# Performance work log

Hardware: AMD Instinct MI355X
Metric: run time of the kernel (lower is better)

The kernel has to match this reference:

```python
import jax, jax.numpy as jnp
import numpy as np

K = 10  # knn neighbors
GF = 100  # gf_num = 25*4


def setup_inputs() -> dict:
    key = jax.random.key(0)
    ks = jax.random.split(key, 14)
    B, N = 4, 8192
    s = 0.1
    inp = {
        "x": jax.random.normal(ks[0], (B, N, 3), dtype=jnp.float32),
        # conv1: (3+K)->20->GF, 1x1 convs == per-point linears
        "w1a": jax.random.normal(ks[1], (3 + K, 20), jnp.float32) * s,
        "b1a": jax.random.normal(ks[2], (20,), jnp.float32) * s,
        "w1b": jax.random.normal(ks[3], (20, GF), jnp.float32) * s,
        "b1b": jax.random.normal(ks[4], (GF,), jnp.float32) * s,
        # conv2: GF->GF
        "w2": jax.random.normal(ks[5], (GF, GF), jnp.float32) * s,
        "b2": jax.random.normal(ks[6], (GF,), jnp.float32) * s,
        # conv3: 2*GF->20->10->2
        "w3a": jax.random.normal(ks[7], (2 * GF, 20), jnp.float32) * s,
        "b3a": jax.random.normal(ks[8], (20,), jnp.float32) * s,
        "w3b": jax.random.normal(ks[9], (20, 10), jnp.float32) * s,
        "b3b": jax.random.normal(ks[10], (10,), jnp.float32) * s,
        "w3c": jax.random.normal(ks[11], (10, 2), jnp.float32) * s,
        "b3c": jax.random.normal(ks[12], (2,), jnp.float32) * s,
    }
    return inp


def reference(x, w1a, b1a, w1b, b1b, w2, b2, w3a, b3a, w3b, b3b, w3c, b3c):
    # pairwise squared distances: [B, N, N]
    sq = jnp.sum(x * x, axis=-1)
    d = sq[:, :, None] + sq[:, None, :] - 2.0 * jnp.einsum("bnc,bmc->bnm", x, x)
    # k smallest distances per point, ascending order (matches torch topk largest=False)
    topk = -jax.lax.top_k(-d, K)[0]  # [B, N, K]
    h = jnp.concatenate([x, topk], axis=-1)  # [B, N, 3+K]
    # conv1 (1x1 convs == per-point linears)
    x1 = jax.nn.relu(jax.nn.relu(h @ w1a + b1a) @ w1b + b1b)  # [B, N, GF]
    # conv2
    x2 = jax.nn.relu(x1 @ w2 + b2)  # [B, N, GF]
    # global avg pool over points, broadcast back
    pool = jnp.mean(x2, axis=1, keepdims=True)  # [B, 1, GF]
    N = x1.shape[1]
    feat = jnp.concatenate([x1, jnp.broadcast_to(pool, (x1.shape[0], N, pool.shape[-1]))], axis=-1)
    # conv3 head + log-softmax over the 2 classes (torch dim=-2 on [B,2,N] layout)
    o = jax.nn.relu(feat @ w3a + b3a)
    o = jax.nn.relu(o @ w3b + b3b)
    o = o @ w3c + b3c  # [B, N, 2]
    return jax.nn.log_softmax(o, axis=-1)
```

## Files before the change

kernel.cpp:

```cpp
#include <hip/hip_runtime.h>
#include <math.h>

#define N_PTS   8192
#define NBATCH  4
#define NQ      (N_PTS*NBATCH)
#define GFN     100
#define KNN     10
#define NSPLIT  8
#define SPLITL  (N_PTS/NSPLIT)
#define MBLK    128
#define CHK     25

__device__ __forceinline__ float med3f(float a, float b, float c){
  return __builtin_amdgcn_fmed3f(a, b, c);
}

__device__ __forceinline__ void insert10(float (&m)[KNN], float d){
  #pragma unroll
  for (int k = KNN-1; k > 0; k--) m[k] = med3f(d, m[k-1], m[k]);
  m[0] = fminf(m[0], d);
}

__global__ __launch_bounds__(256) void knn_kernel(const float* __restrict__ x,
                                                  float* __restrict__ cand,
                                                  float* __restrict__ pool){
  __shared__ float4 tile[SPLITL];
  const int t  = threadIdx.x;
  const int qb = blockIdx.x;
  const int s  = blockIdx.y;
  const int q  = qb * 256 + t;
  const int b  = q >> 13;
  const float* xb = x + (size_t)b * N_PTS * 3;

  if (qb == 0 && s == 0){
    for (int i = t; i < NBATCH*GFN; i += 256) pool[i] = 0.0f;
  }

  #pragma unroll
  for (int k = 0; k < 4; k++){
    const int j = t + 256*k;
    const float* ps = xb + (size_t)(s*SPLITL + j)*3;
    float px = ps[0], py = ps[1], pz = ps[2];
    float sq = fmaf(pz, pz, fmaf(py, py, px*px));
    tile[j] = make_float4(px, py, pz, sq);
  }
  __syncthreads();

  const float xi = x[(size_t)q*3+0], yi = x[(size_t)q*3+1], zi = x[(size_t)q*3+2];
  const float sqi = fmaf(zi, zi, fmaf(yi, yi, xi*xi));

  float m[KNN];
  #pragma unroll
  for (int k = 0; k < KNN; k++) m[k] = INFINITY;

  #pragma unroll 8
  for (int j = 0; j < SPLITL; j++){
    float4 p = tile[j];
    float dot = fmaf(zi, p.z, fmaf(yi, p.y, xi*p.x));
    float d   = fmaf(-2.0f, dot, sqi + p.w);
    insert10(m, d);
  }

  #pragma unroll
  for (int k = 0; k < KNN; k++) cand[(size_t)(s*KNN + k)*NQ + q] = m[k];
}

__global__ __launch_bounds__(256) void mlp1_kernel(
    const float* __restrict__ x,   const float* __restrict__ cand,
    const float* __restrict__ w1a, const float* __restrict__ b1a,
    const float* __restrict__ w1b, const float* __restrict__ b1b,
    const float* __restrict__ w2,  const float* __restrict__ b2,
    float* __restrict__ x1t, float* __restrict__ pool){
  __shared__ float t20s[MBLK*21];
  __shared__ float x1s[MBLK*101];
  const int t = threadIdx.x;
  const int p = t & 63;
  const int g = __builtin_amdgcn_readfirstlane(t >> 6);
  const int q0 = blockIdx.x * MBLK;
  const int b  = q0 >> 13;

  if (g < 2){
    const int pr = g*64 + p;
    const int q  = q0 + pr;
    float m[KNN];
    #pragma unroll
    for (int k = 0; k < KNN; k++) m[k] = INFINITY;
    #pragma unroll
    for (int i = 0; i < NSPLIT*KNN; i++) insert10(m, cand[(size_t)i*NQ + q]);

    float h[13];
    h[0] = x[(size_t)q*3+0]; h[1] = x[(size_t)q*3+1]; h[2] = x[(size_t)q*3+2];
    #pragma unroll
    for (int k = 0; k < KNN; k++) h[3+k] = m[k];

    float a[20];
    #pragma unroll
    for (int o = 0; o < 20; o++) a[o] = b1a[o];
    #pragma unroll
    for (int c = 0; c < 13; c++){
      float hv = h[c];
      #pragma unroll
      for (int o = 0; o < 20; o++) a[o] = fmaf(hv, w1a[c*20+o], a[o]);
    }
    #pragma unroll
    for (int o = 0; o < 20; o++) t20s[pr*21 + o] = fmaxf(a[o], 0.0f);
  }
  __syncthreads();

  const int o0 = g * CHK;
  float accA[CHK], accB[CHK];

  #pragma unroll
  for (int k = 0; k < CHK; k++){ float bv = b1b[o0+k]; accA[k] = bv; accB[k] = bv; }
  #pragma unroll 4
  for (int c = 0; c < 20; c++){
    float ta = t20s[p*21 + c];
    float tb = t20s[(64+p)*21 + c];
    #pragma unroll
    for (int k = 0; k < CHK; k++){
      float w = w1b[c*GFN + o0 + k];
      accA[k] = fmaf(ta, w, accA[k]);
      accB[k] = fmaf(tb, w, accB[k]);
    }
  }
  #pragma unroll
  for (int k = 0; k < CHK; k++){
    float va = fmaxf(accA[k], 0.0f);
    float vb = fmaxf(accB[k], 0.0f);
    x1s[p*101 + o0 + k] = va;
    x1s[(64+p)*101 + o0 + k] = vb;
    x1t[(size_t)(o0+k)*NQ + q0 + p]      = va;
    x1t[(size_t)(o0+k)*NQ + q0 + 64 + p] = vb;
  }
  __syncthreads();

  #pragma unroll
  for (int k = 0; k < CHK; k++){ float bv = b2[o0+k]; accA[k] = bv; accB[k] = bv; }
  #pragma unroll 4
  for (int c = 0; c < GFN; c++){
    float xa = x1s[p*101 + c];
    float xb = x1s[(64+p)*101 + c];
    #pragma unroll
    for (int k = 0; k < CHK; k++){
      float w = w2[c*GFN + o0 + k];
      accA[k] = fmaf(xa, w, accA[k]);
      accB[k] = fmaf(xb, w, accB[k]);
    }
  }
  #pragma unroll
  for (int k = 0; k < CHK; k++){
    float va = fmaxf(accA[k], 0.0f);
    float vb = fmaxf(accB[k], 0.0f);
    #pragma unroll
    for (int off = 1; off < 64; off <<= 1){
      va += __shfl_xor(va, off);
      vb += __shfl_xor(vb, off);
    }
    if (p == 0){
      atomicAdd(&pool[b*GFN + o0 + k], va);
      atomicAdd(&pool[b*GFN + o0 + k], vb);
    }
  }
}

__global__ __launch_bounds__(128) void head_kernel(
    const float* __restrict__ x1t, const float* __restrict__ pool,
    const float* __restrict__ w3a, const float* __restrict__ b3a,
    const float* __restrict__ w3b, const float* __restrict__ b3b,
    const float* __restrict__ w3c, const float* __restrict__ b3c,
    float* __restrict__ out){
  __shared__ float poolm[GFN];
  __shared__ float poolpart[20];
  const int t = threadIdx.x;
  const int q = blockIdx.x * 128 + t;
  const int b = q >> 13;

  if (t < GFN) poolm[t] = pool[b*GFN+t] * (1.0f / (float)N_PTS);
  __syncthreads();
  if (t < 20){
    float a = b3a[t];
    for (int c = 0; c < GFN; c++) a = fmaf(poolm[c], w3a[(GFN+c)*20+t], a);
    poolpart[t] = a;
  }
  __syncthreads();

  float acc[20];
  #pragma unroll
  for (int o = 0; o < 20; o++) acc[o] = 0.0f;
  #pragma unroll 8
  for (int c = 0; c < GFN; c++){
    float xv = x1t[(size_t)c*NQ + q];
    #pragma unroll
    for (int o = 0; o < 20; o++) acc[o] = fmaf(xv, w3a[c*20+o], acc[o]);
  }
  float o1[20];
  #pragma unroll
  for (int o = 0; o < 20; o++) o1[o] = fmaxf(acc[o] + poolpart[o], 0.0f);

  float o2[10];
  #pragma unroll
  for (int o = 0; o < 10; o++){
    float a = b3b[o];
    #pragma unroll
    for (int c = 0; c < 20; c++) a = fmaf(o1[c], w3b[c*10+o], a);
    o2[o] = fmaxf(a, 0.0f);
  }
  float e0 = b3c[0], e1 = b3c[1];
  #pragma unroll
  for (int c = 0; c < 10; c++){
    e0 = fmaf(o2[c], w3c[c*2+0], e0);
    e1 = fmaf(o2[c], w3c[c*2+1], e1);
  }
  float mx = fmaxf(e0, e1);
  float a0 = e0 - mx, a1 = e1 - mx;
  float lse = logf(expf(a0) + expf(a1));
  float2 r; r.x = a0 - lse; r.y = a1 - lse;
  *reinterpret_cast<float2*>(out + (size_t)q*2) = r;
}

extern "C" void kernel_launch(void* const* d_in, const int* in_sizes, int n_in,
                              void* d_out, int out_size, void* d_ws, size_t ws_size,
                              hipStream_t stream) {
  const float* x   = (const float*)d_in[0];
  const float* w1a = (const float*)d_in[1];
  const float* b1a = (const float*)d_in[2];
  const float* w1b = (const float*)d_in[3];
  const float* b1b = (const float*)d_in[4];
  const float* w2  = (const float*)d_in[5];
  const float* b2  = (const float*)d_in[6];
  const float* w3a = (const float*)d_in[7];
  const float* b3a = (const float*)d_in[8];
  const float* w3b = (const float*)d_in[9];
  const float* b3b = (const float*)d_in[10];
  const float* w3c = (const float*)d_in[11];
  const float* b3c = (const float*)d_in[12];
  float* out = (float*)d_out;

  char* ws = (char*)d_ws;
  float* cand = (float*)ws;
  float* x1t  = (float*)(ws + (size_t)NQ*NSPLIT*KNN*4);
  float* pool = (float*)(ws + (size_t)NQ*NSPLIT*KNN*4
                            + (size_t)GFN*NQ*4);

  knn_kernel<<<dim3(NQ/256, NSPLIT), 256, 0, stream>>>(x, cand, pool);
  mlp1_kernel<<<NQ/MBLK, 256, 0, stream>>>(x, cand, w1a, b1a, w1b, b1b, w2, b2, x1t, pool);
  head_kernel<<<NQ/128, 128, 0, stream>>>(x1t, pool, w3a, b3a, w3b, b3b, w3c, b3c, out);
}
```

Before: 273.3 us.

## Register-block KNN queries, widen MLP block, store x1 row-major for head

The KNN kernel now has each thread handle 4 query points against a shared tile, so every LDS load of a reference point is reused four times. The split count doubles to 16 so the grid stays large. The MLP kernel runs 512 threads, one point per thread-row with software-prefetched w2 weights, and writes x1 row-major so the head kernel can read it with float4 loads. The costs are more registers per thread in KNN (40 running minima), twice the candidate buffer traffic, and a longer merge loop in the MLP kernel.

```diff
diff --git a/kernel.cpp b/kernel.cpp
--- a/kernel.cpp
+++ b/kernel.cpp
@@ -6,10 +6,10 @@
 #define NQ      (N_PTS*NBATCH)
 #define GFN     100
 #define KNN     10
-#define NSPLIT  8
+#define NSPLIT  16
 #define SPLITL  (N_PTS/NSPLIT)
+#define QPL     4
 #define MBLK    128
-#define CHK     25
 
 __device__ __forceinline__ float med3f(float a, float b, float c){
   return __builtin_amdgcn_fmed3f(a, b, c);
@@ -25,52 +25,68 @@
                                                   float* __restrict__ cand,
                                                   float* __restrict__ pool){
   __shared__ float4 tile[SPLITL];
-  const int t  = threadIdx.x;
-  const int qb = blockIdx.x;
-  const int s  = blockIdx.y;
-  const int q  = qb * 256 + t;
-  const int b  = q >> 13;
+  const int t   = threadIdx.x;
+  const int w   = t >> 6;
+  const int p   = t & 63;
+  const int s   = blockIdx.y;
+  const int qb0 = blockIdx.x * 1024;
+  const int b   = qb0 >> 13;
   const float* xb = x + (size_t)b * N_PTS * 3;
 
-  if (qb == 0 && s == 0){
+  if (blockIdx.x == 0 && s == 0){
     for (int i = t; i < NBATCH*GFN; i += 256) pool[i] = 0.0f;
   }
 
   #pragma unroll
-  for (int k = 0; k < 4; k++){
+  for (int k = 0; k < 2; k++){
     const int j = t + 256*k;
     const float* ps = xb + (size_t)(s*SPLITL + j)*3;
     float px = ps[0], py = ps[1], pz = ps[2];
-    float sq = fmaf(pz, pz, fmaf(py, py, px*px));
-    tile[j] = make_float4(px, py, pz, sq);
-  }
-  __syncthreads();
-
-  const float xi = x[(size_t)q*3+0], yi = x[(size_t)q*3+1], zi = x[(size_t)q*3+2];
-  const float sqi = fmaf(zi, zi, fmaf(yi, yi, xi*xi));
-
-  float m[KNN];
-  #pragma unroll
-  for (int k = 0; k < KNN; k++) m[k] = INFINITY;
-
-  #pragma unroll 8
+    tile[j] = make_float4(px, py, pz, fmaf(pz, pz, fmaf(py, py, px*px)));
+  }
+  __syncthreads();
+
+  float qx[QPL], qy[QPL], qz[QPL], qs[QPL];
+  #pragma unroll
+  for (int u = 0; u < QPL; u++){
+    const int q = qb0 + w*256 + u*64 + p;
+    qx[u] = x[(size_t)q*3+0];
+    qy[u] = x[(size_t)q*3+1];
+    qz[u] = x[(size_t)q*3+2];
+    qs[u] = fmaf(qz[u], qz[u], fmaf(qy[u], qy[u], qx[u]*qx[u]));
+  }
+
+  float m[QPL][KNN];
+  #pragma unroll
+  for (int u = 0; u < QPL; u++)
+    #pragma unroll
+    for (int k = 0; k < KNN; k++) m[u][k] = INFINITY;
+
+  #pragma unroll 4
   for (int j = 0; j < SPLITL; j++){
-    float4 p = tile[j];
-    float dot = fmaf(zi, p.z, fmaf(yi, p.y, xi*p.x));
-    float d   = fmaf(-2.0f, dot, sqi + p.w);
-    insert10(m, d);
-  }
-
-  #pragma unroll
-  for (int k = 0; k < KNN; k++) cand[(size_t)(s*KNN + k)*NQ + q] = m[k];
-}
-
-__global__ __launch_bounds__(256) void mlp1_kernel(
+    float4 pt = tile[j];
+    #pragma unroll
+    for (int u = 0; u < QPL; u++){
+      float dot = fmaf(qz[u], pt.z, fmaf(qy[u], pt.y, qx[u]*pt.x));
+      float d   = fmaf(-2.0f, dot, qs[u] + pt.w);
+      insert10(m[u], d);
+    }
+  }
+
+  #pragma unroll
+  for (int u = 0; u < QPL; u++){
+    const int q = qb0 + w*256 + u*64 + p;
+    #pragma unroll
+    for (int k = 0; k < KNN; k++) cand[(size_t)(s*KNN + k)*NQ + q] = m[u][k];
+  }
+}
+
+__global__ __launch_bounds__(512) void mlp1_kernel(
     const float* __restrict__ x,   const float* __restrict__ cand,
     const float* __restrict__ w1a, const float* __restrict__ b1a,
     const float* __restrict__ w1b, const float* __restrict__ b1b,
     const float* __restrict__ w2,  const float* __restrict__ b2,
-    float* __restrict__ x1t, float* __restrict__ pool){
+    float* __restrict__ x1r, float* __restrict__ pool){
   __shared__ float t20s[MBLK*21];
   __shared__ float x1s[MBLK*101];
   const int t = threadIdx.x;
@@ -85,7 +101,7 @@
     float m[KNN];
     #pragma unroll
     for (int k = 0; k < KNN; k++) m[k] = INFINITY;
-    #pragma unroll
+    #pragma unroll 4
     for (int i = 0; i < NSPLIT*KNN; i++) insert10(m, cand[(size_t)i*NQ + q]);
 
     float h[13];
@@ -107,64 +123,61 @@
   }
   __syncthreads();
 
-  const int o0 = g * CHK;
-  float accA[CHK], accB[CHK];
-
-  #pragma unroll
-  for (int k = 0; k < CHK; k++){ float bv = b1b[o0+k]; accA[k] = bv; accB[k] = bv; }
-  #pragma unroll 4
+  const int half = g >> 2;
+  const int ph   = half*64 + p;
+  const int q    = q0 + ph;
+  const int o0   = (g & 3) * 25;
+
+  float acc[25];
+
+  #pragma unroll
+  for (int k = 0; k < 25; k++) acc[k] = b1b[o0+k];
+  #pragma unroll 1
   for (int c = 0; c < 20; c++){
-    float ta = t20s[p*21 + c];
-    float tb = t20s[(64+p)*21 + c];
-    #pragma unroll
-    for (int k = 0; k < CHK; k++){
-      float w = w1b[c*GFN + o0 + k];
-      accA[k] = fmaf(ta, w, accA[k]);
-      accB[k] = fmaf(tb, w, accB[k]);
+    float tv = t20s[ph*21 + c];
+    #pragma unroll
+    for (int k = 0; k < 25; k++) acc[k] = fmaf(tv, w1b[c*GFN + o0 + k], acc[k]);
+  }
+  #pragma unroll
+  for (int k = 0; k < 25; k++){
+    float v = fmaxf(acc[k], 0.0f);
+    x1s[ph*101 + o0 + k] = v;
+    x1r[(size_t)q*GFN + o0 + k] = v;
+  }
+  __syncthreads();
+
+  float wA[25], wB[25];
+  #pragma unroll
+  for (int k = 0; k < 25; k++) acc[k] = b2[o0+k];
+  #pragma unroll
+  for (int k = 0; k < 25; k++) wA[k] = w2[o0 + k];
+  #pragma unroll 1
+  for (int c = 0; c < GFN; c += 2){
+    #pragma unroll
+    for (int k = 0; k < 25; k++) wB[k] = w2[(c+1)*GFN + o0 + k];
+    float xv = x1s[ph*101 + c];
+    #pragma unroll
+    for (int k = 0; k < 25; k++) acc[k] = fmaf(xv, wA[k], acc[k]);
+    if (c + 2 < GFN){
+      #pragma unroll
+      for (int k = 0; k < 25; k++) wA[k] = w2[(c+2)*GFN + o0 + k];
     }
-  }
-  #pragma unroll
-  for (int k = 0; k < CHK; k++){
-    float va = fmaxf(accA[k], 0.0f);
-    float vb = fmaxf(accB[k], 0.0f);
-    x1s[p*101 + o0 + k] = va;
-    x1s[(64+p)*101 + o0 + k] = vb;
-    x1t[(size_t)(o0+k)*NQ + q0 + p]      = va;
-    x1t[(size_t)(o0+k)*NQ + q0 + 64 + p] = vb;
-  }
-  __syncthreads();
-
-  #pragma unroll
-  for (int k = 0; k < CHK; k++){ float bv = b2[o0+k]; accA[k] = bv; accB[k] = bv; }
-  #pragma unroll 4
-  for (int c = 0; c < GFN; c++){
-    float xa = x1s[p*101 + c];
-    float xb = x1s[(64+p)*101 + c];
-    #pragma unroll
-    for (int k = 0; k < CHK; k++){
-      float w = w2[c*GFN + o0 + k];
-      accA[k] = fmaf(xa, w, accA[k]);
-      accB[k] = fmaf(xb, w, accB[k]);
-    }
-  }
-  #pragma unroll
-  for (int k = 0; k < CHK; k++){
-    float va = fmaxf(accA[k], 0.0f);
-    float vb = fmaxf(accB[k], 0.0f);
-    #pragma unroll
-    for (int off = 1; off < 64; off <<= 1){
-      va += __shfl_xor(va, off);
-      vb += __shfl_xor(vb, off);
-    }
-    if (p == 0){
-      atomicAdd(&pool[b*GFN + o0 + k], va);
-      atomicAdd(&pool[b*GFN + o0 + k], vb);
-    }
+    xv = x1s[ph*101 + c + 1];
+    #pragma unroll
+    for (int k = 0; k < 25; k++) acc[k] = fmaf(xv, wB[k], acc[k]);
+  }
+
+  #pragma unroll
+  for (int k = 0; k < 25; k++){
+    float v = fmaxf(acc[k], 0.0f);
+    #pragma unroll
+    for (int off = 1; off < 64; off <<= 1) v += __shfl_xor(v, off);
+    if (p == 0) atomicAdd(&pool[b*GFN + o0 + k], v);
   }
 }
 
 __global__ __launch_bounds__(128) void head_kernel(
-    const float* __restrict__ x1t, const float* __restrict__ pool,
+    const float* __restrict__ x1r, const float* __restrict__ pool,
     const float* __restrict__ w3a, const float* __restrict__ b3a,
     const float* __restrict__ w3b, const float* __restrict__ b3b,
     const float* __restrict__ w3c, const float* __restrict__ b3c,
@@ -187,11 +200,19 @@
   float acc[20];
   #pragma unroll
   for (int o = 0; o < 20; o++) acc[o] = 0.0f;
-  #pragma unroll 8
-  for (int c = 0; c < GFN; c++){
-    float xv = x1t[(size_t)c*NQ + q];
-    #pragma unroll
-    for (int o = 0; o < 20; o++) acc[o] = fmaf(xv, w3a[c*20+o], acc[o]);
+  const float4* xr = reinterpret_cast<const float4*>(x1r + (size_t)q*GFN);
+  #pragma unroll 5
+  for (int c4 = 0; c4 < 25; c4++){
+    float4 v = xr[c4];
+    const float* wr = w3a + c4*4*20;
+    #pragma unroll
+    for (int o = 0; o < 20; o++) acc[o] = fmaf(v.x, wr[o],    acc[o]);
+    #pragma unroll
+    for (int o = 0; o < 20; o++) acc[o] = fmaf(v.y, wr[20+o], acc[o]);
+    #pragma unroll
+    for (int o = 0; o < 20; o++) acc[o] = fmaf(v.z, wr[40+o], acc[o]);
+    #pragma unroll
+    for (int o = 0; o < 20; o++) acc[o] = fmaf(v.w, wr[60+o], acc[o]);
   }
   float o1[20];
   #pragma unroll
@@ -238,11 +259,11 @@
 
   char* ws = (char*)d_ws;
   float* cand = (float*)ws;
-  float* x1t  = (float*)(ws + (size_t)NQ*NSPLIT*KNN*4);
+  float* x1r  = (float*)(ws + (size_t)NQ*NSPLIT*KNN*4);
   float* pool = (float*)(ws + (size_t)NQ*NSPLIT*KNN*4
-                            + (size_t)GFN*NQ*4);
-
-  knn_kernel<<<dim3(NQ/256, NSPLIT), 256, 0, stream>>>(x, cand, pool);
-  mlp1_kernel<<<NQ/MBLK, 256, 0, stream>>>(x, cand, w1a, b1a, w1b, b1b, w2, b2, x1t, pool);
-  head_kernel<<<NQ/128, 128, 0, stream>>>(x1t, pool, w3a, b3a, w3b, b3b, w3c, b3c, out);
-}
+                            + (size_t)NQ*GFN*4);
+
+  knn_kernel<<<dim3(NQ/1024, NSPLIT), 256, 0, stream>>>(x, cand, pool);
+  mlp1_kernel<<<NQ/MBLK, 512, 0, stream>>>(x, cand, w1a, b1a, w1b, b1b, w2, b2, x1r, pool);
+  head_kernel<<<NQ/128, 128, 0, stream>>>(x1r, pool, w3a, b3a, w3b, b3b, w3c, b3c, out);
+}
```

New measurement: 292.9 us. 7.2% more time.
